# Performance work log

Hardware: AMD Instinct MI355X
Metric: run time of the kernel (lower is better)

The kernel has to match this reference:

```python
import jax, jax.numpy as jnp
import numpy as np

D = 128  # embedding dimension (init arg d)

def setup_inputs() -> dict:
    key = jax.random.key(0)
    x = jax.random.uniform(key, (256, 4096), dtype=jnp.float32)  # (b, n) in [0,1]
    return {"x": x}

def reference(x) -> jnp.ndarray:
    # Fourier basis: emb[b, n, i] = cos(pi * i * x[b, n]), i = 0..D-1
    i = jnp.arange(D, dtype=x.dtype)  # (D,)
    emb = jnp.cos(jnp.pi * x[..., None] * i)  # (b, n, D)
    return emb
```

## Files before the change

kernel.cpp:

```cpp
#include <hip/hip_runtime.h>


constexpr int D = 128;

__global__ __launch_bounds__(256) void Emb_37967510896970_kernel(
    const float* __restrict__ x, float4* __restrict__ out, int total_rows)
{
    const int tx  = threadIdx.x & 31;
    const int ty  = threadIdx.x >> 5;
    const int rpb = 256 >> 5;
    const float i0 = (float)(tx << 2);

    for (int row = blockIdx.x * rpb + ty; row < total_rows;
         row += (int)gridDim.x * rpb) {
        const float h = 0.5f * x[row];
        float4 v;
        v.x = __builtin_amdgcn_cosf(__builtin_amdgcn_fractf(h * i0));
        v.y = __builtin_amdgcn_cosf(__builtin_amdgcn_fractf(h * (i0 + 1.0f)));
        v.z = __builtin_amdgcn_cosf(__builtin_amdgcn_fractf(h * (i0 + 2.0f)));
        v.w = __builtin_amdgcn_cosf(__builtin_amdgcn_fractf(h * (i0 + 3.0f)));
        out[(size_t)row * (D / 4) + tx] = v;
    }
}

extern "C" void kernel_launch(void* const* d_in, const int* in_sizes, int n_in,
                              void* d_out, int out_size, void* d_ws, size_t ws_size,
                              hipStream_t stream) {
    const float* x = (const float*)d_in[0];
    float4* out = (float4*)d_out;
    const int total_rows = in_sizes[0];
    const int rpb = 8;
    int grid = (total_rows + rpb - 1) / rpb;
    if (grid > 2048) grid = 2048;
    Emb_37967510896970_kernel<<<grid, 256, 0, stream>>>(x, out, total_rows);
}
```

Before: 125.5 us.

## Compute 16 contiguous cosines per thread with nontemporal stores and full grid

Each thread now produces 16 consecutive outputs (four 16-byte vectors) of one row instead of 4, and writes them with nontemporal stores. The grid-stride loop capped at 2048 blocks is replaced by one thread per 16 outputs across the whole tensor. The intent is to raise bytes in flight per thread and keep the write-only output from polluting cache on this store-bound kernel. In exchange, each thread's four stores are strided by 64 bytes across lanes rather than fully contiguous per instruction, which may reduce coalescing.

```diff
diff --git a/kernel.cpp b/kernel.cpp
--- a/kernel.cpp
+++ b/kernel.cpp
@@ -1,36 +1,42 @@
 #include <hip/hip_runtime.h>
 
 
-constexpr int D = 128;
+typedef float f32x4 __attribute__((ext_vector_type(4)));
 
 __global__ __launch_bounds__(256) void Emb_37967510896970_kernel(
-    const float* __restrict__ x, float4* __restrict__ out, int total_rows)
+    const float* __restrict__ x, f32x4* __restrict__ out, long long total_elems)
 {
-    const int tx  = threadIdx.x & 31;
-    const int ty  = threadIdx.x >> 5;
-    const int rpb = 256 >> 5;
-    const float i0 = (float)(tx << 2);
+    const long long tid = (long long)blockIdx.x * 256 + threadIdx.x;
+    if (tid * 16 >= total_elems) return;
 
-    for (int row = blockIdx.x * rpb + ty; row < total_rows;
-         row += (int)gridDim.x * rpb) {
-        const float h = 0.5f * x[row];
-        float4 v;
-        v.x = __builtin_amdgcn_cosf(__builtin_amdgcn_fractf(h * i0));
-        v.y = __builtin_amdgcn_cosf(__builtin_amdgcn_fractf(h * (i0 + 1.0f)));
-        v.z = __builtin_amdgcn_cosf(__builtin_amdgcn_fractf(h * (i0 + 2.0f)));
-        v.w = __builtin_amdgcn_cosf(__builtin_amdgcn_fractf(h * (i0 + 3.0f)));
-        out[(size_t)row * (D / 4) + tx] = v;
+    const int row = (int)(tid >> 3);
+    const int sub = (int)tid & 7;
+    const float h  = 0.5f * x[row];
+    const float hb = h * (float)(sub << 4);
+
+    f32x4 v[4];
+#pragma unroll
+    for (int q = 0; q < 4; ++q) {
+#pragma unroll
+        for (int k = 0; k < 4; ++k) {
+            float ang = fmaf(h, (float)(4 * q + k), hb);
+            v[q][k] = __builtin_amdgcn_cosf(__builtin_amdgcn_fractf(ang));
+        }
     }
+
+    f32x4* p = out + tid * 4;
+#pragma unroll
+    for (int q = 0; q < 4; ++q)
+        __builtin_nontemporal_store(v[q], p + q);
 }
 
 extern "C" void kernel_launch(void* const* d_in, const int* in_sizes, int n_in,
                               void* d_out, int out_size, void* d_ws, size_t ws_size,
                               hipStream_t stream) {
     const float* x = (const float*)d_in[0];
-    float4* out = (float4*)d_out;
-    const int total_rows = in_sizes[0];
-    const int rpb = 8;
-    int grid = (total_rows + rpb - 1) / rpb;
-    if (grid > 2048) grid = 2048;
-    Emb_37967510896970_kernel<<<grid, 256, 0, stream>>>(x, out, total_rows);
+    f32x4* out = (f32x4*)d_out;
+    const long long total_elems = (long long)out_size;
+    const long long threads = (total_elems + 15) / 16;
+    const int grid = (int)((threads + 255) / 256);
+    Emb_37967510896970_kernel<<<grid, 256, 0, stream>>>(x, out, total_elems);
 }
```

Result: slower. 416.0 us (+231.4%).
